# Kernel tuning notes

Hardware: AMD Instinct MI355X
Metric: run time of the kernel (lower is better)

## Reference

```python
import jax, jax.numpy as jnp
import numpy as np

INIT_SCALE = 5

def _steps(n_full):
    half = [i + 1 for i in range(0, int(n_full) + 1, 2)]
    return list(reversed(half[1:])) + half

STEP_H = np.array(_steps(192 / INIT_SCALE), dtype=np.float32)  # len 39
STEP_W = np.array(_steps(256 / INIT_SCALE), dtype=np.float32)  # len 51
MASK_H, MASK_W = len(STEP_H), len(STEP_W)


def _prelu(x, a):
    return jnp.maximum(x, 0.0) + a * jnp.minimum(x, 0.0)


def _reduce(x, w, b, a):
    # Conv2dBlock(64,4,1,1,norm='none',activation='prelu'): activation BEFORE 1x1 conv (per source)
    return jnp.einsum('nchw,oc->nohw', _prelu(x, a), w) + b[None, :, None, None]


def _crop_coords(cx, cy, H, W):
    # replicates floor(center - mask/2) / floor(center + mask/2) + border clamping
    top = cy - (MASK_H + 1) // 2
    bottom = cy + MASK_H // 2
    left = cx - (MASK_W + 1) // 2
    right = cx + MASK_W // 2
    dy1 = jnp.maximum(-top, 0)
    dy2 = jnp.maximum(bottom - H, 0)
    dx1 = jnp.maximum(-left, 0)
    dx2 = jnp.maximum(right - W, 0)
    new_top = top + dy1
    new_left = left + dx1
    new_h = jnp.maximum(bottom - dy2 - new_top, 0)
    new_w = jnp.maximum(right - dx2 - new_left, 0)
    return new_top, new_left, new_h, new_w, dy1, dx1


def _gimg(img, rows, cols):  # img (C,H,W) -> (C,len(rows),len(cols))
    return img[:, rows[:, None], cols[None, :]]


def _gmask(m, rows, cols):  # m (MASK_H,MASK_W)
    return m[rows[:, None], cols[None, :]]


def _forward(location, fea_c, fea_p, scale_param, H, W, c_landmark, p_landmark, w1, b1, a1, w2, b2, a2):
    N = fea_c.shape[0]
    ratio = H // fea_c.shape[2]
    fea_cn = _reduce(jnp.repeat(jnp.repeat(fea_c, ratio, 2), ratio, 3), w1, b1, a1)
    fea_pn = _reduce(jnp.repeat(jnp.repeat(fea_p, ratio, 2), ratio, 3), w2, b2, a2)
    C = fea_cn.shape[1]

    init_h = W / INIT_SCALE  # note: swapped vs H/W, exactly as in the original forward
    init_w = H / INIT_SCALE
    sig = jax.nn.sigmoid
    adj_cw, adj_ch = scale_param[:, :, 0, 0], scale_param[:, :, 0, 1]
    adj_pw, adj_ph = scale_param[:, :, 1, 0], scale_param[:, :, 1, 1]
    step_h = jnp.asarray(STEP_H)
    step_w = jnp.asarray(STEP_W)

    def box_mask(adj_h, adj_w):
        h = (init_h * sig(adj_h))[..., None]  # (N,32,1)
        w = (init_w * sig(adj_w))[..., None]
        return sig((h - step_h) * 2)[..., :, None] * sig((w - step_w) * 2)[..., None, :]

    src_mask = box_mask(adj_ch, adj_cw)  # (N,32,39,51)
    tar_mask = box_mask(adj_ph, adj_pw)

    r_ar = jnp.arange(MASK_H, dtype=jnp.int32)
    c_ar = jnp.arange(MASK_W, dtype=jnp.int32)
    c_cx, c_cy = c_landmark[:, :, 0], c_landmark[:, :, 1]
    p_cx, p_cy = p_landmark[:, :, 0], p_landmark[:, :, 1]
    use_lm = ~(((c_cx == 0) & (c_cy == 0)) | ((p_cx == 0) & (p_cy == 0)))  # (N,32)

    def make_patch(fea, lm_mask, cx, cy):
        top, left, nh, nw, dy1, dx1 = _crop_coords(cx, cy, H, W)
        rows = jnp.clip(top[..., None] + r_ar, 0, H - 1)        # (N,32,39)
        cols = jnp.clip(left[..., None] + c_ar, 0, W - 1)       # (N,32,51)
        mrows = jnp.clip(dy1[..., None] + r_ar, 0, MASK_H - 1)
        mcols = jnp.clip(dx1[..., None] + c_ar, 0, MASK_W - 1)
        valid = (use_lm[..., None, None]
                 & (r_ar[None, None, :, None] < nh[..., None, None])
                 & (c_ar[None, None, None, :] < nw[..., None, None]))  # (N,32,39,51)
        g = jax.vmap(lambda f, R, Cc: jax.vmap(_gimg, in_axes=(None, 0, 0))(f, R, Cc))(fea, rows, cols)  # (N,32,C,39,51)
        m = jax.vmap(jax.vmap(_gmask))(lm_mask, mrows, mcols)  # (N,32,39,51)
        patch = jnp.where(valid[:, :, None], g * m[:, :, None], 0.0)
        return patch, rows, cols, valid

    cloth, rows_c, cols_c, valid_c = make_patch(fea_cn, src_mask, c_cx, c_cy)
    person, rows_p, cols_p, valid_p = make_patch(fea_pn, tar_mask, p_cx, p_cy)

    loc5 = location.reshape(N, 32, 2, H, W)
    loc_g = jax.vmap(jax.vmap(_gimg))(loc5, rows_c, cols_c)  # (N,32,2,39,51)
    loc_patch = jnp.where(valid_c[:, :, None], loc_g, -1.0)  # -1 fill as in source

    L = MASK_H * MASK_W
    P = person.reshape(N, 32, C, L)
    K = cloth.reshape(N, 32, C, L)
    V = loc_patch.reshape(N, 32, 2, L)
    scores = jnp.einsum('nicp,nicq->nipq', P, K)  # (N,32,L,L) query=person px, key=cloth px
    corr = jax.nn.softmax(scores, axis=-1)
    flow_patch = jnp.einsum('nipq,nidq->nidp', corr, V).reshape(N, 32, 2, MASK_H, MASK_W)

    # scatter person-crop regions back into full-res outputs (invalid -> dump row/col H,W)
    rr = jnp.where(valid_p, jnp.broadcast_to(rows_p[:, :, :, None], valid_p.shape), H)
    cc = jnp.where(valid_p, jnp.broadcast_to(cols_p[:, :, None, :], valid_p.shape), W)
    bb = jnp.arange(N)[:, None, None, None]
    ii = jnp.arange(32)[None, :, None, None]
    flow_pad = jnp.full((N, 32, H + 1, W + 1, 2), -1.0, dtype=flow_patch.dtype)
    flow_pad = flow_pad.at[bb, ii, rr, cc].set(flow_patch.transpose(0, 1, 3, 4, 2))
    landmark_flow = flow_pad[:, :, :H, :W, :].transpose(0, 1, 4, 2, 3).reshape(N, 64, H, W)
    mask = jnp.zeros((N, 32, H + 1, W + 1), dtype=flow_patch.dtype).at[bb, ii, rr, cc].set(1.0)[:, :, :H, :W]
    return landmark_flow, mask


def setup_inputs() -> dict:
    key = jax.random.key(0)
    ks = jax.random.split(key, 8)
    N, H, W = 1, 192, 256
    fh, fw = H // 4, W // 4
    return {
        'location': jax.random.normal(ks[0], (N, 64, H, W), jnp.float32),
        'fea_c': jax.random.normal(ks[1], (N, 64, fh, fw), jnp.float32),
        'fea_p': jax.random.normal(ks[2], (N, 64, fh, fw), jnp.float32),
        'scale_param': jax.random.normal(ks[3], (N, 32, 2, 2), jnp.float32),
        'H': H,
        'W': W,
        'c_landmark': jax.random.randint(ks[4], (N, 32, 2), 0, 180, jnp.int32),
        'p_landmark': jax.random.randint(ks[5], (N, 32, 2), 0, 180, jnp.int32),
        'w1': jax.random.normal(ks[6], (4, 64), jnp.float32) * 0.05,
        'b1': jnp.zeros((4,), jnp.float32),
        'a1': jnp.array(0.25, jnp.float32),
        'w2': jax.random.normal(ks[7], (4, 64), jnp.float32) * 0.05,
        'b2': jnp.zeros((4,), jnp.float32),
        'a2': jnp.array(0.25, jnp.float32),
    }


def reference(location, fea_c, fea_p, scale_param, H, W, c_landmark, p_landmark, w1, b1, a1, w2, b2, a2):
    return _forward(location, fea_c, fea_p, scale_param, H, W, c_landmark, p_landmark, w1, b1, a1, w2, b2, a2)
```

## Files before the change

### kernel.cpp

```cpp
#include <hip/hip_runtime.h>

constexpr int kH = 192, kW = 256, kHW = kH * kW;
constexpr int kFH = 48, kFW = 64, kFHW = kFH * kFW;
constexpr int kMH = 39, kMW = 51;
constexpr int kL = kMH * kMW;
constexpr int kLP = 2048;
constexpr int kHeads = 32;
constexpr float kInitH = 256.0f / 5.0f;
constexpr float kInitW = 192.0f / 5.0f;
constexpr float kL2E = 1.44269504088896340736f;
constexpr float kBias = -16.0f;
constexpr float kPadCorr = 59.0f / 65536.0f;

typedef float v2f __attribute__((ext_vector_type(2)));
__device__ __forceinline__ v2f pkfma(v2f a, v2f b, v2f c) {
  return __builtin_elementwise_fma(a, b, c);
}

__device__ __forceinline__ float fast_exp2(float x) {
#if __has_builtin(__builtin_amdgcn_exp2f)
  return __builtin_amdgcn_exp2f(x);
#else
  float r;
  asm("v_exp_f32 %0, %1\n\ts_nop 1" : "=v"(r) : "v"(x));
  return r;
#endif
}

struct HeadParams {
  int use;
  int ntop_c, nleft_c, nh_c, nw_c, dy1_c, dx1_c;
  int ntop_p, nleft_p, nh_p, nw_p, dy1_p, dx1_p;
  float h_c, w_c, h_p, w_p;
};

__device__ __forceinline__ float sigf(float x) { return 1.0f / (1.0f + __expf(-x)); }
__device__ __forceinline__ float stepH(int j) { return (float)(2 * abs(j - 19) + 1); }
__device__ __forceinline__ float stepW(int j) { return (float)(2 * abs(j - 25) + 1); }

__device__ void headParams(int i, const int* clm, const int* plm, const float* sp, HeadParams& h) {
  int ccx = clm[2 * i], ccy = clm[2 * i + 1];
  int pcx = plm[2 * i], pcy = plm[2 * i + 1];
  h.use = !(((ccx == 0) && (ccy == 0)) || ((pcx == 0) && (pcy == 0)));
  {
    int top = ccy - (kMH + 1) / 2, bottom = ccy + kMH / 2;
    int left = ccx - (kMW + 1) / 2, right = ccx + kMW / 2;
    int dy1 = max(-top, 0), dy2 = max(bottom - kH, 0);
    int dx1 = max(-left, 0), dx2 = max(right - kW, 0);
    h.ntop_c = top + dy1; h.nleft_c = left + dx1; h.dy1_c = dy1; h.dx1_c = dx1;
    h.nh_c = max(kMH - dy1 - dy2, 0); h.nw_c = max(kMW - dx1 - dx2, 0);
  }
  {
    int top = pcy - (kMH + 1) / 2, bottom = pcy + kMH / 2;
    int left = pcx - (kMW + 1) / 2, right = pcx + kMW / 2;
    int dy1 = max(-top, 0), dy2 = max(bottom - kH, 0);
    int dx1 = max(-left, 0), dx2 = max(right - kW, 0);
    h.ntop_p = top + dy1; h.nleft_p = left + dx1; h.dy1_p = dy1; h.dx1_p = dx1;
    h.nh_p = max(kMH - dy1 - dy2, 0); h.nw_p = max(kMW - dx1 - dx2, 0);
  }
  float adj_cw = sp[4 * i + 0], adj_ch = sp[4 * i + 1];
  float adj_pw = sp[4 * i + 2], adj_ph = sp[4 * i + 3];
  h.h_c = kInitH * sigf(adj_ch);
  h.w_c = kInitW * sigf(adj_cw);
  h.h_p = kInitH * sigf(adj_ph);
  h.w_p = kInitW * sigf(adj_pw);
}

__device__ __forceinline__ float4 conv4(const float* __restrict__ f, const float* __restrict__ w,
                                        const float* __restrict__ b, float a, int fpix, float s) {
  float acc0 = 0.f, acc1 = 0.f, acc2 = 0.f, acc3 = 0.f;
#pragma unroll 8
  for (int c = 0; c < 64; ++c) {
    float x = f[c * kFHW + fpix];
    float pr = fmaxf(x, 0.f) + a * fminf(x, 0.f);
    acc0 = fmaf(pr, w[c], acc0);
    acc1 = fmaf(pr, w[64 + c], acc1);
    acc2 = fmaf(pr, w[128 + c], acc2);
    acc3 = fmaf(pr, w[192 + c], acc3);
  }
  return make_float4((acc0 + b[0]) * s, (acc1 + b[1]) * s, (acc2 + b[2]) * s, (acc3 + b[3]) * s);
}

__global__ void k_patch(const float* __restrict__ fc, const float* __restrict__ fp,
                        const float* __restrict__ w1, const float* __restrict__ b1, const float* __restrict__ a1,
                        const float* __restrict__ w2, const float* __restrict__ b2, const float* __restrict__ a2,
                        const float* __restrict__ loc,
                        const float* __restrict__ sp, const int* __restrict__ clm, const int* __restrict__ plm,
                        float* __restrict__ Rec, float4* __restrict__ Pall,
                        int* __restrict__ hpws) {
  __shared__ int shp[20];
  int i = blockIdx.y;
  if (threadIdx.x == 0) {
    HeadParams h; headParams(i, clm, plm, sp, h);
    shp[0] = h.use;
    shp[1] = h.ntop_c; shp[2] = h.nleft_c; shp[3] = h.nh_c; shp[4] = h.nw_c; shp[5] = h.dy1_c; shp[6] = h.dx1_c;
    shp[7] = h.ntop_p; shp[8] = h.nleft_p; shp[9] = h.nh_p; shp[10] = h.nw_p; shp[11] = h.dy1_p; shp[12] = h.dx1_p;
    shp[13] = __float_as_int(h.h_c); shp[14] = __float_as_int(h.w_c);
    shp[15] = __float_as_int(h.h_p); shp[16] = __float_as_int(h.w_p);
    if (blockIdx.x == 0) {
      int* o = hpws + i * 20;
#pragma unroll
      for (int t = 0; t < 17; ++t) o[t] = shp[t];
    }
  }
  __syncthreads();
  int use = shp[0];
  int ntop_c = shp[1], nleft_c = shp[2], nh_c = shp[3], nw_c = shp[4], dy1_c = shp[5], dx1_c = shp[6];
  int ntop_p = shp[7], nleft_p = shp[8], nh_p = shp[9], nw_p = shp[10], dy1_p = shp[11], dx1_p = shp[12];
  float h_c = __int_as_float(shp[13]), w_c = __int_as_float(shp[14]);
  float h_p = __int_as_float(shp[15]), w_p = __int_as_float(shp[16]);

  int q = blockIdx.x * 256 + threadIdx.x;
  int qr = q / kMW, qc = q - qr * kMW;
  float a1v = a1[0], a2v = a2[0];
  {
    bool val = (q < kL) && use && (qr < nh_c) && (qc < nw_c);
    int row = min(ntop_c + qr, kH - 1);
    int col = min(nleft_c + qc, kW - 1);
    int mr = min(dy1_c + qr, kMH - 1);
    int mc = min(dx1_c + qc, kMW - 1);
    float mv = sigf((h_c - stepH(mr)) * 2.f) * sigf((w_c - stepW(mc)) * 2.f);
    int fpix = (row >> 2) * kFW + (col >> 2);
    float kx = 0.f, ky = 0.f, kz = 0.f, kw = 0.f, vx = -1.f, vy = -1.f;
    if (val) {
      float4 k = conv4(fc, w1, b1, a1v, fpix, mv);
      kx = k.x; ky = k.y; kz = k.z; kw = k.w;
      vx = loc[(2 * i) * kHW + row * kW + col];
      vy = loc[(2 * i + 1) * kHW + row * kW + col];
    }
    float* r = Rec + (size_t)(i * (kLP / 2) + (q >> 1)) * 12 + (q & 1);
    r[0] = kx; r[2] = ky; r[4] = kz; r[6] = kw; r[8] = vx; r[10] = vy;
  }
  if (q < kL) {
    bool val = use && (qr < nh_p) && (qc < nw_p);
    int row = min(ntop_p + qr, kH - 1);
    int col = min(nleft_p + qc, kW - 1);
    int mr = min(dy1_p + qr, kMH - 1);
    int mc = min(dx1_p + qc, kMW - 1);
    float mv = sigf((h_p - stepH(mr)) * 2.f) * sigf((w_p - stepW(mc)) * 2.f) * kL2E;
    int fpix = (row >> 2) * kFW + (col >> 2);
    float4 pv = make_float4(0.f, 0.f, 0.f, 0.f);
    if (val) pv = conv4(fp, w2, b2, a2v, fpix, mv);
    Pall[i * kL + q] = pv;
  }
}

template<int QLEN>
__global__ void __launch_bounds__(256) k_attn_t(const float* __restrict__ Rec,
                                                const float4* __restrict__ Pall,
                                                float4* __restrict__ pPart) {
  int i = blockIdx.z;
  int qsi = blockIdx.y;
  int p = blockIdx.x * 249 + threadIdx.x;
  int pe = min(p, kL - 1);
  const float* rec = Rec + (size_t)(i * (kLP / 2) + qsi * (QLEN / 2)) * 12;
  float4 P = Pall[i * kL + pe];
  v2f PX = {P.x, P.x}, PY = {P.y, P.y}, PZ = {P.z, P.z}, PW = {P.w, P.w};
  const v2f B = {kBias, kBias};
  v2f dA = {0.f, 0.f}, dB = {0.f, 0.f};
  v2f xA = {0.f, 0.f}, xB = {0.f, 0.f};
  v2f yA = {0.f, 0.f}, yB = {0.f, 0.f};
#pragma unroll 8
  for (int t = 0; t < QLEN / 2; t += 2) {
    const float* rA = rec + t * 12;
    const float* rB = rA + 12;
    v2f sA = pkfma(PW, *(const v2f*)(rA + 6), B);
    sA = pkfma(PZ, *(const v2f*)(rA + 4), sA);
    sA = pkfma(PY, *(const v2f*)(rA + 2), sA);
    sA = pkfma(PX, *(const v2f*)(rA + 0), sA);
    v2f sB = pkfma(PW, *(const v2f*)(rB + 6), B);
    sB = pkfma(PZ, *(const v2f*)(rB + 4), sB);
    sB = pkfma(PY, *(const v2f*)(rB + 2), sB);
    sB = pkfma(PX, *(const v2f*)(rB + 0), sB);
    v2f eA = {fast_exp2(sA.x), fast_exp2(sA.y)};
    v2f eB = {fast_exp2(sB.x), fast_exp2(sB.y)};
    dA += eA;
    xA = pkfma(eA, *(const v2f*)(rA + 8), xA);
    yA = pkfma(eA, *(const v2f*)(rA + 10), yA);
    dB += eB;
    xB = pkfma(eB, *(const v2f*)(rB + 8), xB);
    yB = pkfma(eB, *(const v2f*)(rB + 10), yB);
  }
  pPart[(i * gridDim.y + qsi) * kLP + pe] =
      make_float4(dA.x + dA.y + dB.x + dB.y,
                  xA.x + xA.y + xB.x + xB.y,
                  yA.x + yA.y + yB.x + yB.y, 0.f);
}

__global__ void k_merge_full(const float4* __restrict__ pPart, int QS,
                             const int* __restrict__ hpws, float* __restrict__ out) {
  int i = blockIdx.y;
  int pix = blockIdx.x * 256 + threadIdx.x;
  const int* hp = hpws + i * 20;
  int use = hp[0];
  int ntop_p = hp[7], nleft_p = hp[8], nh_p = hp[9], nw_p = hp[10];
  int r = pix >> 8;
  int c = pix & 255;
  int pr = r - ntop_p, pc = c - nleft_p;
  bool val = use && ((unsigned)pr < (unsigned)nh_p) && ((unsigned)pc < (unsigned)nw_p);
  float f0 = -1.f, f1 = -1.f, mk = 0.f;
  if (val) {
    int p = pr * kMW + pc;
    float den = -kPadCorr, n0 = kPadCorr, n1 = kPadCorr;
    for (int k = 0; k < QS; ++k) {
      float4 t = pPart[(i * QS + k) * kLP + p];
      den += t.x; n0 += t.y; n1 += t.z;
    }
    float inv = 1.0f / den;
    f0 = n0 * inv; f1 = n1 * inv; mk = 1.0f;
  }
  out[(2 * i) * kHW + pix]      = f0;
  out[(2 * i + 1) * kHW + pix]  = f1;
  out[64 * kHW + i * kHW + pix] = mk;
}

extern "C" void kernel_launch(void* const* d_in, const int* in_sizes, int n_in,
                              void* d_out, int out_size, void* d_ws, size_t ws_size,
                              hipStream_t stream) {
  (void)in_sizes; (void)n_in; (void)out_size;
  const float* loc = (const float*)d_in[0];
  const float* fc  = (const float*)d_in[1];
  const float* fp  = (const float*)d_in[2];
  const float* sp  = (const float*)d_in[3];
  const int* clm   = (const int*)d_in[6];
  const int* plm   = (const int*)d_in[7];
  const float* w1  = (const float*)d_in[8];
  const float* b1  = (const float*)d_in[9];
  const float* a1  = (const float*)d_in[10];
  const float* w2  = (const float*)d_in[11];
  const float* b2  = (const float*)d_in[12];
  const float* a2  = (const float*)d_in[13];
  float* out = (float*)d_out;
  char* ws = (char*)d_ws;

  int*    hpws = (int*)(ws);
  float*  Rec  = (float*)(ws + 4096);
  float4* Pall = (float4*)(ws + 1576960);
  size_t base = 2595328;
  size_t perQS = (size_t)kHeads * kLP * 16;
  int QS = 1;
  if (ws_size >= base + 16 * perQS) QS = 16;
  else if (ws_size >= base + 8 * perQS) QS = 8;
  else if (ws_size >= base + 4 * perQS) QS = 4;
  else if (ws_size >= base + 2 * perQS) QS = 2;
  float4* pPart = (float4*)(ws + base);

  k_patch<<<dim3(kLP / 256, kHeads), 256, 0, stream>>>(fc, fp, w1, b1, a1, w2, b2, a2,
                                                       loc, sp, clm, plm, Rec, Pall, hpws);
  dim3 ag(8, QS, kHeads);
  switch (QS) {
    case 16: k_attn_t<128><<<ag, 256, 0, stream>>>(Rec, Pall, pPart); break;
    case 8:  k_attn_t<256><<<ag, 256, 0, stream>>>(Rec, Pall, pPart); break;
    case 4:  k_attn_t<512><<<ag, 256, 0, stream>>>(Rec, Pall, pPart); break;
    case 2:  k_attn_t<1024><<<ag, 256, 0, stream>>>(Rec, Pall, pPart); break;
    default: k_attn_t<2048><<<ag, 256, 0, stream>>>(Rec, Pall, pPart); break;
  }
  k_merge_full<<<dim3(kHW / 256, kHeads), 256, 0, stream>>>(pPart, QS, hpws, out);
}
```

Measured before the change: 56.58 us.

## Compute patch attention with bf16 split-precision MFMA instead of packed FP32 FMA

Replaces the scalar/packed-FMA attention kernel with one built on 16x16x16 bf16 MFMA. The QK scores use a hi/lo bf16 split (three MFMAs) and the value accumulation uses two MFMAs. k_patch now writes K, P and V tiles in MFMA fragment layout, with extra blocks building the V tile including a ones row for the denominator. The merge kernel reduces two fixed halves instead of a workspace-dependent split count. The intent is to move the dominant quadratic work onto matrix cores. The cost is extra conversion work and a bf16 rounding of the exponentials, which reduces accuracy.

```diff
diff --git a/kernel.cpp b/kernel.cpp
--- a/kernel.cpp
+++ b/kernel.cpp
@@ -6,25 +6,44 @@
 constexpr int kL = kMH * kMW;
 constexpr int kLP = 2048;
 constexpr int kHeads = 32;
+constexpr int kPT = 128;
 constexpr float kInitH = 256.0f / 5.0f;
 constexpr float kInitW = 192.0f / 5.0f;
 constexpr float kL2E = 1.44269504088896340736f;
 constexpr float kBias = -16.0f;
 constexpr float kPadCorr = 59.0f / 65536.0f;
 
-typedef float v2f __attribute__((ext_vector_type(2)));
-__device__ __forceinline__ v2f pkfma(v2f a, v2f b, v2f c) {
-  return __builtin_elementwise_fma(a, b, c);
+typedef unsigned long long u64;
+typedef short s4 __attribute__((ext_vector_type(4)));
+typedef float f4 __attribute__((ext_vector_type(4)));
+
+__device__ __forceinline__ s4 u2s(u64 x) { union { u64 u; s4 s; } c; c.u = x; return c.s; }
+
+__device__ __forceinline__ f4 mfma16(s4 a, s4 b, f4 c) {
+#if __has_builtin(__builtin_amdgcn_mfma_f32_16x16x16bf16_1k)
+  return __builtin_amdgcn_mfma_f32_16x16x16bf16_1k(a, b, c, 0, 0, 0);
+#else
+  f4 d;
+  asm("v_mfma_f32_16x16x16_bf16 %0, %1, %2, %3" : "=v"(d) : "v"(a), "v"(b), "v"(c));
+  return d;
+#endif
 }
 
 __device__ __forceinline__ float fast_exp2(float x) {
 #if __has_builtin(__builtin_amdgcn_exp2f)
   return __builtin_amdgcn_exp2f(x);
 #else
-  float r;
-  asm("v_exp_f32 %0, %1\n\ts_nop 1" : "=v"(r) : "v"(x));
-  return r;
+  float r; asm("v_exp_f32 %0, %1\n\ts_nop 1" : "=v"(r) : "v"(x)); return r;
 #endif
+}
+
+__device__ __forceinline__ unsigned f2bfu(float f) {
+  unsigned u = __float_as_uint(f);
+  return (u + 0x7FFFu + ((u >> 16) & 1u)) >> 16;
+}
+__device__ __forceinline__ float bfuf(unsigned h) { return __uint_as_float(h << 16); }
+__device__ __forceinline__ u64 pack4(unsigned h0, unsigned h1, unsigned h2, unsigned h3) {
+  return (u64)(h0 | (h1 << 16)) | ((u64)(h2 | (h3 << 16)) << 32);
 }
 
 struct HeadParams {
@@ -43,16 +62,16 @@
   int pcx = plm[2 * i], pcy = plm[2 * i + 1];
   h.use = !(((ccx == 0) && (ccy == 0)) || ((pcx == 0) && (pcy == 0)));
   {
-    int top = ccy - (kMH + 1) / 2, bottom = ccy + kMH / 2;
-    int left = ccx - (kMW + 1) / 2, right = ccx + kMW / 2;
+    int top = ccy - 20, bottom = ccy + 19;
+    int left = ccx - 26, right = ccx + 25;
     int dy1 = max(-top, 0), dy2 = max(bottom - kH, 0);
     int dx1 = max(-left, 0), dx2 = max(right - kW, 0);
     h.ntop_c = top + dy1; h.nleft_c = left + dx1; h.dy1_c = dy1; h.dx1_c = dx1;
     h.nh_c = max(kMH - dy1 - dy2, 0); h.nw_c = max(kMW - dx1 - dx2, 0);
   }
   {
-    int top = pcy - (kMH + 1) / 2, bottom = pcy + kMH / 2;
-    int left = pcx - (kMW + 1) / 2, right = pcx + kMW / 2;
+    int top = pcy - 20, bottom = pcy + 19;
+    int left = pcx - 26, right = pcx + 25;
     int dy1 = max(-top, 0), dy2 = max(bottom - kH, 0);
     int dx1 = max(-left, 0), dx2 = max(right - kW, 0);
     h.ntop_p = top + dy1; h.nleft_p = left + dx1; h.dy1_p = dy1; h.dx1_p = dx1;
@@ -81,113 +100,166 @@
   return make_float4((acc0 + b[0]) * s, (acc1 + b[1]) * s, (acc2 + b[2]) * s, (acc3 + b[3]) * s);
 }
 
+__device__ __forceinline__ void split4(float4 v, u64& hi, u64& lo) {
+  unsigned h0 = f2bfu(v.x), h1 = f2bfu(v.y), h2 = f2bfu(v.z), h3 = f2bfu(v.w);
+  unsigned l0 = f2bfu(v.x - bfuf(h0)), l1 = f2bfu(v.y - bfuf(h1));
+  unsigned l2 = f2bfu(v.z - bfuf(h2)), l3 = f2bfu(v.w - bfuf(h3));
+  hi = pack4(h0, h1, h2, h3);
+  lo = pack4(l0, l1, l2, l3);
+}
+
 __global__ void k_patch(const float* __restrict__ fc, const float* __restrict__ fp,
                         const float* __restrict__ w1, const float* __restrict__ b1, const float* __restrict__ a1,
                         const float* __restrict__ w2, const float* __restrict__ b2, const float* __restrict__ a2,
                         const float* __restrict__ loc,
                         const float* __restrict__ sp, const int* __restrict__ clm, const int* __restrict__ plm,
-                        float* __restrict__ Rec, float4* __restrict__ Pall,
+                        u64* __restrict__ Ph, u64* __restrict__ Pl,
+                        u64* __restrict__ Kh, u64* __restrict__ Kl,
+                        u64* __restrict__ Vh, u64* __restrict__ Vl,
                         int* __restrict__ hpws) {
-  __shared__ int shp[20];
   int i = blockIdx.y;
-  if (threadIdx.x == 0) {
-    HeadParams h; headParams(i, clm, plm, sp, h);
-    shp[0] = h.use;
-    shp[1] = h.ntop_c; shp[2] = h.nleft_c; shp[3] = h.nh_c; shp[4] = h.nw_c; shp[5] = h.dy1_c; shp[6] = h.dx1_c;
-    shp[7] = h.ntop_p; shp[8] = h.nleft_p; shp[9] = h.nh_p; shp[10] = h.nw_p; shp[11] = h.dy1_p; shp[12] = h.dx1_p;
-    shp[13] = __float_as_int(h.h_c); shp[14] = __float_as_int(h.w_c);
-    shp[15] = __float_as_int(h.h_p); shp[16] = __float_as_int(h.w_p);
-    if (blockIdx.x == 0) {
-      int* o = hpws + i * 20;
+  int bx = blockIdx.x;
+  if (bx < 8) {
+    __shared__ int shp[20];
+    if (threadIdx.x == 0) {
+      HeadParams h; headParams(i, clm, plm, sp, h);
+      shp[0] = h.use;
+      shp[1] = h.ntop_c; shp[2] = h.nleft_c; shp[3] = h.nh_c; shp[4] = h.nw_c; shp[5] = h.dy1_c; shp[6] = h.dx1_c;
+      shp[7] = h.ntop_p; shp[8] = h.nleft_p; shp[9] = h.nh_p; shp[10] = h.nw_p; shp[11] = h.dy1_p; shp[12] = h.dx1_p;
+      shp[13] = __float_as_int(h.h_c); shp[14] = __float_as_int(h.w_c);
+      shp[15] = __float_as_int(h.h_p); shp[16] = __float_as_int(h.w_p);
+      if (bx == 0) {
+        int* o = hpws + i * 20;
 #pragma unroll
-      for (int t = 0; t < 17; ++t) o[t] = shp[t];
+        for (int t = 0; t < 17; ++t) o[t] = shp[t];
+      }
     }
-  }
-  __syncthreads();
-  int use = shp[0];
-  int ntop_c = shp[1], nleft_c = shp[2], nh_c = shp[3], nw_c = shp[4], dy1_c = shp[5], dx1_c = shp[6];
-  int ntop_p = shp[7], nleft_p = shp[8], nh_p = shp[9], nw_p = shp[10], dy1_p = shp[11], dx1_p = shp[12];
-  float h_c = __int_as_float(shp[13]), w_c = __int_as_float(shp[14]);
-  float h_p = __int_as_float(shp[15]), w_p = __int_as_float(shp[16]);
-
-  int q = blockIdx.x * 256 + threadIdx.x;
-  int qr = q / kMW, qc = q - qr * kMW;
-  float a1v = a1[0], a2v = a2[0];
-  {
-    bool val = (q < kL) && use && (qr < nh_c) && (qc < nw_c);
-    int row = min(ntop_c + qr, kH - 1);
-    int col = min(nleft_c + qc, kW - 1);
-    int mr = min(dy1_c + qr, kMH - 1);
-    int mc = min(dx1_c + qc, kMW - 1);
-    float mv = sigf((h_c - stepH(mr)) * 2.f) * sigf((w_c - stepW(mc)) * 2.f);
-    int fpix = (row >> 2) * kFW + (col >> 2);
-    float kx = 0.f, ky = 0.f, kz = 0.f, kw = 0.f, vx = -1.f, vy = -1.f;
-    if (val) {
-      float4 k = conv4(fc, w1, b1, a1v, fpix, mv);
-      kx = k.x; ky = k.y; kz = k.z; kw = k.w;
-      vx = loc[(2 * i) * kHW + row * kW + col];
-      vy = loc[(2 * i + 1) * kHW + row * kW + col];
+    __syncthreads();
+    int use = shp[0];
+    int ntop_c = shp[1], nleft_c = shp[2], nh_c = shp[3], nw_c = shp[4], dy1_c = shp[5], dx1_c = shp[6];
+    int ntop_p = shp[7], nleft_p = shp[8], nh_p = shp[9], nw_p = shp[10], dy1_p = shp[11], dx1_p = shp[12];
+    float h_c = __int_as_float(shp[13]), w_c = __int_as_float(shp[14]);
+    float h_p = __int_as_float(shp[15]), w_p = __int_as_float(shp[16]);
+
+    int q = bx * 256 + threadIdx.x;
+    int qr = q / kMW, qc = q - qr * kMW;
+    int fi = (i * kPT + (q >> 4)) * 16 + (q & 15);
+    {
+      bool val = (q < kL) && use && (qr < nh_c) && (qc < nw_c);
+      float4 kv = make_float4(0.f, 0.f, 0.f, 0.f);
+      if (val) {
+        int row = min(ntop_c + qr, kH - 1);
+        int col = min(nleft_c + qc, kW - 1);
+        int mr = min(dy1_c + qr, kMH - 1);
+        int mc = min(dx1_c + qc, kMW - 1);
+        float mv = sigf((h_c - stepH(mr)) * 2.f) * sigf((w_c - stepW(mc)) * 2.f);
+        int fpix = (row >> 2) * kFW + (col >> 2);
+        kv = conv4(fc, w1, b1, a1[0], fpix, mv);
+      }
+      u64 hi, lo; split4(kv, hi, lo);
+      Kh[fi] = hi; Kl[fi] = lo;
     }
-    float* r = Rec + (size_t)(i * (kLP / 2) + (q >> 1)) * 12 + (q & 1);
-    r[0] = kx; r[2] = ky; r[4] = kz; r[6] = kw; r[8] = vx; r[10] = vy;
-  }
-  if (q < kL) {
-    bool val = use && (qr < nh_p) && (qc < nw_p);
-    int row = min(ntop_p + qr, kH - 1);
-    int col = min(nleft_p + qc, kW - 1);
-    int mr = min(dy1_p + qr, kMH - 1);
-    int mc = min(dx1_p + qc, kMW - 1);
-    float mv = sigf((h_p - stepH(mr)) * 2.f) * sigf((w_p - stepW(mc)) * 2.f) * kL2E;
-    int fpix = (row >> 2) * kFW + (col >> 2);
-    float4 pv = make_float4(0.f, 0.f, 0.f, 0.f);
-    if (val) pv = conv4(fp, w2, b2, a2v, fpix, mv);
-    Pall[i * kL + q] = pv;
-  }
-}
-
-template<int QLEN>
-__global__ void __launch_bounds__(256) k_attn_t(const float* __restrict__ Rec,
-                                                const float4* __restrict__ Pall,
-                                                float4* __restrict__ pPart) {
-  int i = blockIdx.z;
-  int qsi = blockIdx.y;
-  int p = blockIdx.x * 249 + threadIdx.x;
-  int pe = min(p, kL - 1);
-  const float* rec = Rec + (size_t)(i * (kLP / 2) + qsi * (QLEN / 2)) * 12;
-  float4 P = Pall[i * kL + pe];
-  v2f PX = {P.x, P.x}, PY = {P.y, P.y}, PZ = {P.z, P.z}, PW = {P.w, P.w};
-  const v2f B = {kBias, kBias};
-  v2f dA = {0.f, 0.f}, dB = {0.f, 0.f};
-  v2f xA = {0.f, 0.f}, xB = {0.f, 0.f};
-  v2f yA = {0.f, 0.f}, yB = {0.f, 0.f};
-#pragma unroll 8
-  for (int t = 0; t < QLEN / 2; t += 2) {
-    const float* rA = rec + t * 12;
-    const float* rB = rA + 12;
-    v2f sA = pkfma(PW, *(const v2f*)(rA + 6), B);
-    sA = pkfma(PZ, *(const v2f*)(rA + 4), sA);
-    sA = pkfma(PY, *(const v2f*)(rA + 2), sA);
-    sA = pkfma(PX, *(const v2f*)(rA + 0), sA);
-    v2f sB = pkfma(PW, *(const v2f*)(rB + 6), B);
-    sB = pkfma(PZ, *(const v2f*)(rB + 4), sB);
-    sB = pkfma(PY, *(const v2f*)(rB + 2), sB);
-    sB = pkfma(PX, *(const v2f*)(rB + 0), sB);
-    v2f eA = {fast_exp2(sA.x), fast_exp2(sA.y)};
-    v2f eB = {fast_exp2(sB.x), fast_exp2(sB.y)};
-    dA += eA;
-    xA = pkfma(eA, *(const v2f*)(rA + 8), xA);
-    yA = pkfma(eA, *(const v2f*)(rA + 10), yA);
-    dB += eB;
-    xB = pkfma(eB, *(const v2f*)(rB + 8), xB);
-    yB = pkfma(eB, *(const v2f*)(rB + 10), yB);
-  }
-  pPart[(i * gridDim.y + qsi) * kLP + pe] =
-      make_float4(dA.x + dA.y + dB.x + dB.y,
-                  xA.x + xA.y + xB.x + xB.y,
-                  yA.x + yA.y + yB.x + yB.y, 0.f);
-}
-
-__global__ void k_merge_full(const float4* __restrict__ pPart, int QS,
+    {
+      bool val = (q < kL) && use && (qr < nh_p) && (qc < nw_p);
+      float4 pv = make_float4(0.f, 0.f, 0.f, 0.f);
+      if (val) {
+        int row = min(ntop_p + qr, kH - 1);
+        int col = min(nleft_p + qc, kW - 1);
+        int mr = min(dy1_p + qr, kMH - 1);
+        int mc = min(dx1_p + qc, kMW - 1);
+        float mv = sigf((h_p - stepH(mr)) * 2.f) * sigf((w_p - stepW(mc)) * 2.f) * kL2E;
+        int fpix = (row >> 2) * kFW + (col >> 2);
+        pv = conv4(fp, w2, b2, a2[0], fpix, mv);
+      }
+      u64 hi, lo; split4(pv, hi, lo);
+      Ph[fi] = hi; Pl[fi] = lo;
+    }
+  } else {
+    int idx = (bx - 8) * 256 + threadIdx.x;
+    int l = idx & 63, qt = idx >> 6;
+    int m = l & 15, g = l >> 4;
+    u64 hi = 0, lo = 0;
+    if (m == 0) {
+      hi = 0x3F803F803F803F80ULL;
+    } else if (m <= 2) {
+      int ccx = clm[2 * i], ccy = clm[2 * i + 1];
+      int pcx = plm[2 * i], pcy = plm[2 * i + 1];
+      int use = !(((ccx == 0) && (ccy == 0)) || ((pcx == 0) && (pcy == 0)));
+      int top = ccy - 20, left = ccx - 26;
+      int dy1 = max(-top, 0), dx1 = max(-left, 0);
+      int dy2 = max(ccy + 19 - kH, 0), dx2 = max(ccx + 25 - kW, 0);
+      int ntop = top + dy1, nleft = left + dx1;
+      int nh = max(kMH - dy1 - dy2, 0), nw = max(kMW - dx1 - dx2, 0);
+      const float* lp = loc + (2 * i + (m - 1)) * kHW;
+#pragma unroll
+      for (int j = 0; j < 4; ++j) {
+        int q = qt * 16 + g * 4 + j;
+        int qr = q / kMW, qc = q - qr * kMW;
+        bool val = (q < kL) && use && (qr < nh) && (qc < nw);
+        int row = min(ntop + qr, kH - 1);
+        int col = min(nleft + qc, kW - 1);
+        float v = val ? lp[row * kW + col] : -1.0f;
+        unsigned hb = f2bfu(v);
+        unsigned lb = f2bfu(v - bfuf(hb));
+        hi |= (u64)hb << (16 * j);
+        lo |= (u64)lb << (16 * j);
+      }
+    }
+    int o = (i * kPT + qt) * 64 + l;
+    Vh[o] = hi; Vl[o] = lo;
+  }
+}
+
+__global__ void __launch_bounds__(256) k_attn_mfma(const u64* __restrict__ Ph, const u64* __restrict__ Pl,
+                                                   const u64* __restrict__ Kh, const u64* __restrict__ Kl,
+                                                   const u64* __restrict__ Vh, const u64* __restrict__ Vl,
+                                                   float4* __restrict__ pPart) {
+  int bid = blockIdx.x;
+  int i = bid >> 6;
+  int r = bid & 63;
+  int h = r & 1;
+  int ptb = (r >> 1) << 2;
+  int wid = threadIdx.x >> 6;
+  int lane = threadIdx.x & 63;
+  int pt = ptb + wid;
+  bool l16 = lane < 16;
+
+  u64 phw = l16 ? Ph[(i * kPT + pt) * 16 + lane] : 0ULL;
+  u64 plw = l16 ? Pl[(i * kPT + pt) * 16 + lane] : 0ULL;
+  s4 bPh = u2s(phw), bPl = u2s(plw);
+
+  int t0 = h * 64;
+  const u64* kh = Kh + (size_t)(i * kPT + t0) * 16;
+  const u64* kl = Kl + (size_t)(i * kPT + t0) * 16;
+  const u64* vh = Vh + (size_t)(i * kPT + t0) * 64;
+  const u64* vl = Vl + (size_t)(i * kPT + t0) * 64;
+
+  f4 acc = {0.f, 0.f, 0.f, 0.f};
+#pragma unroll 4
+  for (int t = 0; t < 64; ++t) {
+    u64 akh = l16 ? kh[t * 16 + lane] : 0ULL;
+    u64 akl = l16 ? kl[t * 16 + lane] : 0ULL;
+    u64 avh = vh[t * 64 + lane];
+    u64 avl = vl[t * 64 + lane];
+    f4 s = {kBias, kBias, kBias, kBias};
+    s = mfma16(u2s(akh), bPl, s);
+    s = mfma16(u2s(akl), bPh, s);
+    s = mfma16(u2s(akh), bPh, s);
+    float e0 = fast_exp2(s.x);
+    float e1 = fast_exp2(s.y);
+    float e2 = fast_exp2(s.z);
+    float e3 = fast_exp2(s.w);
+    u64 eu = pack4(f2bfu(e0), f2bfu(e1), f2bfu(e2), f2bfu(e3));
+    s4 E = u2s(eu);
+    acc = mfma16(u2s(avl), E, acc);
+    acc = mfma16(u2s(avh), E, acc);
+  }
+  if (l16) {
+    pPart[((size_t)(i * kPT + pt) * 2 + h) * 16 + lane] = make_float4(acc.x, acc.y, acc.z, 0.f);
+  }
+}
+
+__global__ void k_merge_full(const float4* __restrict__ pPart,
                              const int* __restrict__ hpws, float* __restrict__ out) {
   int i = blockIdx.y;
   int pix = blockIdx.x * 256 + threadIdx.x;
@@ -201,11 +273,13 @@
   float f0 = -1.f, f1 = -1.f, mk = 0.f;
   if (val) {
     int p = pr * kMW + pc;
-    float den = -kPadCorr, n0 = kPadCorr, n1 = kPadCorr;
-    for (int k = 0; k < QS; ++k) {
-      float4 t = pPart[(i * QS + k) * kLP + p];
-      den += t.x; n0 += t.y; n1 += t.z;
-    }
+    int pt = p >> 4, lq = p & 15;
+    size_t base = ((size_t)(i * kPT + pt) * 2) * 16 + lq;
+    float4 t0 = pPart[base];
+    float4 t1 = pPart[base + 16];
+    float den = t0.x + t1.x - kPadCorr;
+    float n0 = t0.y + t1.y + kPadCorr;
+    float n1 = t0.z + t1.z + kPadCorr;
     float inv = 1.0f / den;
     f0 = n0 * inv; f1 = n1 * inv; mk = 1.0f;
   }
@@ -217,7 +291,7 @@
 extern "C" void kernel_launch(void* const* d_in, const int* in_sizes, int n_in,
                               void* d_out, int out_size, void* d_ws, size_t ws_size,
                               hipStream_t stream) {
-  (void)in_sizes; (void)n_in; (void)out_size;
+  (void)in_sizes; (void)n_in; (void)out_size; (void)ws_size;
   const float* loc = (const float*)d_in[0];
   const float* fc  = (const float*)d_in[1];
   const float* fp  = (const float*)d_in[2];
@@ -233,27 +307,18 @@
   float* out = (float*)d_out;
   char* ws = (char*)d_ws;
 
-  int*    hpws = (int*)(ws);
-  float*  Rec  = (float*)(ws + 4096);
-  float4* Pall = (float4*)(ws + 1576960);
-  size_t base = 2595328;
-  size_t perQS = (size_t)kHeads * kLP * 16;
-  int QS = 1;
-  if (ws_size >= base + 16 * perQS) QS = 16;
-  else if (ws_size >= base + 8 * perQS) QS = 8;
-  else if (ws_size >= base + 4 * perQS) QS = 4;
-  else if (ws_size >= base + 2 * perQS) QS = 2;
-  float4* pPart = (float4*)(ws + base);
-
-  k_patch<<<dim3(kLP / 256, kHeads), 256, 0, stream>>>(fc, fp, w1, b1, a1, w2, b2, a2,
-                                                       loc, sp, clm, plm, Rec, Pall, hpws);
-  dim3 ag(8, QS, kHeads);
-  switch (QS) {
-    case 16: k_attn_t<128><<<ag, 256, 0, stream>>>(Rec, Pall, pPart); break;
-    case 8:  k_attn_t<256><<<ag, 256, 0, stream>>>(Rec, Pall, pPart); break;
-    case 4:  k_attn_t<512><<<ag, 256, 0, stream>>>(Rec, Pall, pPart); break;
-    case 2:  k_attn_t<1024><<<ag, 256, 0, stream>>>(Rec, Pall, pPart); break;
-    default: k_attn_t<2048><<<ag, 256, 0, stream>>>(Rec, Pall, pPart); break;
-  }
-  k_merge_full<<<dim3(kHW / 256, kHeads), 256, 0, stream>>>(pPart, QS, hpws, out);
-}
+  int* hpws = (int*)(ws);
+  u64* Ph   = (u64*)(ws + 4096);
+  u64* Pl   = (u64*)(ws + 528384);
+  u64* Kh   = (u64*)(ws + 1052672);
+  u64* Kl   = (u64*)(ws + 1576960);
+  u64* Vh   = (u64*)(ws + 2101248);
+  u64* Vl   = (u64*)(ws + 4198400);
+  float4* pPart = (float4*)(ws + 6295552);
+
+  k_patch<<<dim3(40, kHeads), 256, 0, stream>>>(fc, fp, w1, b1, a1, w2, b2, a2,
+                                                loc, sp, clm, plm,
+                                                Ph, Pl, Kh, Kl, Vh, Vl, hpws);
+  k_attn_mfma<<<2048, 256, 0, stream>>>(Ph, Pl, Kh, Kl, Vh, Vl, pPart);
+  k_merge_full<<<dim3(kHW / 256, kHeads), 256, 0, stream>>>(pPart, hpws, out);
+}
```

After: 87.56 us. 54.8% more time.
